# Optimization experiments

Hardware: AMD Instinct MI355X
Metric: run time of the kernel (lower is better)

Reference implementation:

```python
import jax, jax.numpy as jnp
import numpy as np

B, CIN, COUT, K = 4096, 128, 128, 9  # batch, in_ch, out_ch, board size / n_offsets


def setup_inputs() -> dict:
    key = jax.random.key(0)
    k1, k2, k3 = jax.random.split(key, 3)
    inputs = jax.random.normal(k1, (B, CIN, K, K), dtype=jnp.float32)   # [B, Cin, 9, 9]
    weights = jax.random.normal(k2, (K, COUT, CIN), dtype=jnp.float32)  # per-offset linear
    bias = jax.random.normal(k3, (K, COUT), dtype=jnp.float32)
    return {"inputs": inputs, "weights": weights, "bias": bias}


def reference(inputs, weights, bias):
    # For each vertical offset k (row of the 9x9 board), gather the slice
    # inputs[:, :, k, :] and apply the k-th linear map plus its bias.
    # out[b, k, oc, x] = sum_i W[k, oc, i] * inputs[b, i, k, x] + bias[k, oc]
    out = jnp.einsum('bikx,koi->bkox', inputs, weights)  # [B, 9, Cout, 9]
    out = out + bias[None, :, :, None]
    return out
```

## Files before the change

kernel.cpp:

```cpp
#include <hip/hip_runtime.h>
#include <hip/hip_bf16.h>


#define NB   4096
#define CINC 128
#define COUTC 128
#define NK   9
#define NX   9
#define BT   16
#define NCOL (BT * NX)
#define LDK  136

typedef __attribute__((ext_vector_type(8))) short short8;
typedef __attribute__((ext_vector_type(4))) float floatx4;
typedef __attribute__((ext_vector_type(2))) float floatx2;

__device__ __forceinline__ short f2bf(float f) {
    union { float f; unsigned u; } v; v.f = f;
    unsigned r = v.u + 0x7fff + ((v.u >> 16) & 1);
    return (short)(r >> 16);
}

__global__ __launch_bounds__(512, 6) void GatherVertical_40656160424516_kernel(
    const float* __restrict__ in, const float* __restrict__ w,
    const float* __restrict__ bias, float* __restrict__ out)
{
    __shared__ __align__(16) char smem[NCOL * LDK * 2];
    short* Il = (short*)smem;

    const int t = threadIdx.x;

    const int j = blockIdx.x;
    const int xcd = j & 7;
    const int slot = j >> 3;
    const int grp = slot / 9;
    const int k = slot - grp * 9;
    const int btile = grp * 8 + xcd;
    const int b0 = btile * BT;

    const int lane = t & 63;
    const int wv = t >> 6;
    const int lc = lane & 15;
    const int quad = lane >> 4;
    const int oc_base = wv * 16;

    const float* wk = w + k * (COUTC * CINC);
    short8 afr[4];
    #pragma unroll
    for (int s = 0; s < 4; ++s) {
        const float* wp = wk + (oc_base + lc) * CINC + s * 32 + quad * 8;
        float4 w0 = *(const float4*)wp;
        float4 w1 = *(const float4*)(wp + 4);
        short8 a;
        a[0] = f2bf(w0.x); a[1] = f2bf(w0.y); a[2] = f2bf(w0.z); a[3] = f2bf(w0.w);
        a[4] = f2bf(w1.x); a[5] = f2bf(w1.y); a[6] = f2bf(w1.z); a[7] = f2bf(w1.w);
        afr[s] = a;
    }

    const float* bk = bias + k * COUTC;
    float bsv[4];
    #pragma unroll
    for (int r = 0; r < 4; ++r) bsv[r] = bk[oc_base + quad * 4 + r];

    const float* inb = in + (size_t)b0 * (CINC * NK * NX) + k * NX;
    #pragma unroll
    for (int it = 0; it < 36; ++it) {
        int f = it * 512 + t;
        int bl = f / (CINC * NX);
        int rem = f - bl * (CINC * NX);
        int i = rem / NX;
        int x = rem - i * NX;
        float v = inb[bl * (CINC * NK * NX) + i * (NK * NX) + x];
        Il[(bl * NX + x) * LDK + i] = f2bf(v);
    }

    __syncthreads();

    floatx4 acc[9];
    #pragma unroll
    for (int n = 0; n < 9; ++n) acc[n] = (floatx4){0.f, 0.f, 0.f, 0.f};

    #pragma unroll
    for (int s = 0; s < 4; ++s) {
        int kof = s * 32 + quad * 8;
        #pragma unroll
        for (int n = 0; n < 9; ++n) {
            short8 bfr = *(const short8*)&Il[(n * 16 + lc) * LDK + kof];
            acc[n] = __builtin_amdgcn_mfma_f32_16x16x32_bf16(afr[s], bfr, acc[n], 0, 0, 0);
        }
    }

    for (int p = 0; p < 2; ++p) {
        __syncthreads();
        float* Ol = (float*)smem;
        #pragma unroll
        for (int n = 0; n < 9; ++n) {
            int nx = n * 16 + lc;
            int bl = nx / 9;
            if ((bl >> 3) == p) {
                int x = nx - bl * 9;
                int base = ((bl & 7) * COUTC + oc_base + quad * 4) * NX + x;
                #pragma unroll
                for (int r = 0; r < 4; ++r)
                    Ol[base + r * NX] = acc[n][r] + bsv[r];
            }
        }
        __syncthreads();
        const float* src = Ol + wv * (COUTC * NX);
        float* dst = out + (size_t)(b0 + p * 8 + wv) * (NK * COUTC * NX)
                         + k * (COUTC * NX);
        #pragma unroll
        for (int s = 0; s < 4; ++s) {
            floatx4 v = *(const floatx4*)(src + s * 256 + lane * 4);
            *(floatx4*)(dst + s * 256 + lane * 4) = v;
        }
        floatx2 v2 = *(const floatx2*)(src + 1024 + lane * 2);
        *(floatx2*)(dst + 1024 + lane * 2) = v2;
    }
}

extern "C" void kernel_launch(void* const* d_in, const int* in_sizes, int n_in,
                              void* d_out, int out_size, void* d_ws, size_t ws_size,
                              hipStream_t stream) {
    const float* in  = (const float*)d_in[0];
    const float* w   = (const float*)d_in[1];
    const float* bs  = (const float*)d_in[2];
    float* out = (float*)d_out;
    dim3 grid((NB / BT) * NK);
    dim3 block(512);
    GatherVertical_40656160424516_kernel<<<grid, block, 0, stream>>>(in, w, bs, out);
}
```

Before: 341.9 us.

## Halve batch tile and use 4 waves each covering two output-channel tiles

Cuts the batch tile from 16 to 8 and the block from 512 to 256 threads. Each wave now holds weight fragments for two 16-row output-channel tiles, so every LDS B fragment feeds two MFMAs. The 72 columns are covered by four full 16-column tiles plus one half-padded tile, and the grid doubles to raise block count and occupancy. In exchange the whole weight slice is reloaded and converted twice as often per batch element, and the padded tile wastes some MFMA work.

```diff
diff --git a/kernel.cpp b/kernel.cpp
--- a/kernel.cpp
+++ b/kernel.cpp
@@ -2,14 +2,16 @@
 #include <hip/hip_bf16.h>
 
 
-#define NB   4096
-#define CINC 128
+#define NB    4096
+#define CINC  128
 #define COUTC 128
-#define NK   9
-#define NX   9
-#define BT   16
-#define NCOL (BT * NX)
-#define LDK  136
+#define NK    9
+#define NX    9
+#define BT    8
+#define NCOL  (BT * NX)
+#define LDK   136
+#define OUTK  (COUTC * NX)
+#define OUTB  (NK * COUTC * NX)
 
 typedef __attribute__((ext_vector_type(8))) short short8;
 typedef __attribute__((ext_vector_type(4))) float floatx4;
@@ -21,12 +23,13 @@
     return (short)(r >> 16);
 }
 
-__global__ __launch_bounds__(512, 6) void GatherVertical_40656160424516_kernel(
+__global__ __launch_bounds__(256, 8) void GatherVertical_40656160424516_kernel(
     const float* __restrict__ in, const float* __restrict__ w,
     const float* __restrict__ bias, float* __restrict__ out)
 {
     __shared__ __align__(16) char smem[NCOL * LDK * 2];
     short* Il = (short*)smem;
+    float* Ol = (float*)smem;
 
     const int t = threadIdx.x;
 
@@ -42,30 +45,32 @@
     const int wv = t >> 6;
     const int lc = lane & 15;
     const int quad = lane >> 4;
-    const int oc_base = wv * 16;
 
     const float* wk = w + k * (COUTC * CINC);
-    short8 afr[4];
+    short8 afr[2][4];
+    float bsv[2][4];
     #pragma unroll
-    for (int s = 0; s < 4; ++s) {
-        const float* wp = wk + (oc_base + lc) * CINC + s * 32 + quad * 8;
-        float4 w0 = *(const float4*)wp;
-        float4 w1 = *(const float4*)(wp + 4);
-        short8 a;
-        a[0] = f2bf(w0.x); a[1] = f2bf(w0.y); a[2] = f2bf(w0.z); a[3] = f2bf(w0.w);
-        a[4] = f2bf(w1.x); a[5] = f2bf(w1.y); a[6] = f2bf(w1.z); a[7] = f2bf(w1.w);
-        afr[s] = a;
+    for (int m = 0; m < 2; ++m) {
+        const int oc_base = wv * 16 + m * 64;
+        #pragma unroll
+        for (int s = 0; s < 4; ++s) {
+            const float* wp = wk + (oc_base + lc) * CINC + s * 32 + quad * 8;
+            float4 w0 = *(const float4*)wp;
+            float4 w1 = *(const float4*)(wp + 4);
+            short8 a;
+            a[0] = f2bf(w0.x); a[1] = f2bf(w0.y); a[2] = f2bf(w0.z); a[3] = f2bf(w0.w);
+            a[4] = f2bf(w1.x); a[5] = f2bf(w1.y); a[6] = f2bf(w1.z); a[7] = f2bf(w1.w);
+            afr[m][s] = a;
+        }
+        const float* bp = bias + k * COUTC + oc_base + quad * 4;
+        #pragma unroll
+        for (int r = 0; r < 4; ++r) bsv[m][r] = bp[r];
     }
-
-    const float* bk = bias + k * COUTC;
-    float bsv[4];
-    #pragma unroll
-    for (int r = 0; r < 4; ++r) bsv[r] = bk[oc_base + quad * 4 + r];
 
     const float* inb = in + (size_t)b0 * (CINC * NK * NX) + k * NX;
     #pragma unroll
     for (int it = 0; it < 36; ++it) {
-        int f = it * 512 + t;
+        int f = it * 256 + t;
         int bl = f / (CINC * NX);
         int rem = f - bl * (CINC * NX);
         int i = rem / NX;
@@ -76,39 +81,46 @@
 
     __syncthreads();
 
-    floatx4 acc[9];
+    floatx4 acc[2][5];
     #pragma unroll
-    for (int n = 0; n < 9; ++n) acc[n] = (floatx4){0.f, 0.f, 0.f, 0.f};
+    for (int m = 0; m < 2; ++m)
+        #pragma unroll
+        for (int n = 0; n < 5; ++n) acc[m][n] = (floatx4){0.f, 0.f, 0.f, 0.f};
 
     #pragma unroll
     for (int s = 0; s < 4; ++s) {
         int kof = s * 32 + quad * 8;
         #pragma unroll
-        for (int n = 0; n < 9; ++n) {
-            short8 bfr = *(const short8*)&Il[(n * 16 + lc) * LDK + kof];
-            acc[n] = __builtin_amdgcn_mfma_f32_16x16x32_bf16(afr[s], bfr, acc[n], 0, 0, 0);
+        for (int n = 0; n < 5; ++n) {
+            int col = (n < 4) ? (n * 16 + lc) : (64 + (lc & 7));
+            short8 bfr = *(const short8*)&Il[col * LDK + kof];
+            acc[0][n] = __builtin_amdgcn_mfma_f32_16x16x32_bf16(afr[0][s], bfr, acc[0][n], 0, 0, 0);
+            acc[1][n] = __builtin_amdgcn_mfma_f32_16x16x32_bf16(afr[1][s], bfr, acc[1][n], 0, 0, 0);
         }
     }
 
     for (int p = 0; p < 2; ++p) {
         __syncthreads();
-        float* Ol = (float*)smem;
         #pragma unroll
-        for (int n = 0; n < 9; ++n) {
+        for (int n = 0; n < 5; ++n) {
             int nx = n * 16 + lc;
+            if (n == 4 && lc >= 8) continue;
             int bl = nx / 9;
-            if ((bl >> 3) == p) {
+            if ((bl >> 2) == p) {
                 int x = nx - bl * 9;
-                int base = ((bl & 7) * COUTC + oc_base + quad * 4) * NX + x;
                 #pragma unroll
-                for (int r = 0; r < 4; ++r)
-                    Ol[base + r * NX] = acc[n][r] + bsv[r];
+                for (int m = 0; m < 2; ++m) {
+                    const int oc_base = wv * 16 + m * 64;
+                    float* op = Ol + ((bl & 3) * COUTC + oc_base + quad * 4) * NX + x;
+                    #pragma unroll
+                    for (int r = 0; r < 4; ++r)
+                        op[r * NX] = acc[m][n][r] + bsv[m][r];
+                }
             }
         }
         __syncthreads();
-        const float* src = Ol + wv * (COUTC * NX);
-        float* dst = out + (size_t)(b0 + p * 8 + wv) * (NK * COUTC * NX)
-                         + k * (COUTC * NX);
+        const float* src = Ol + wv * OUTK;
+        float* dst = out + (size_t)(b0 + p * 4 + wv) * OUTB + k * OUTK;
         #pragma unroll
         for (int s = 0; s < 4; ++s) {
             floatx4 v = *(const floatx4*)(src + s * 256 + lane * 4);
@@ -127,6 +139,6 @@
     const float* bs  = (const float*)d_in[2];
     float* out = (float*)d_out;
     dim3 grid((NB / BT) * NK);
-    dim3 block(512);
+    dim3 block(256);
     GatherVertical_40656160424516_kernel<<<grid, block, 0, stream>>>(in, w, bs, out);
 }
```

New measurement: 512.8 us. 1.5x slower.
